# Performance work log

Measured on AMD Instinct MI355X. Metric: run time of the kernel, lower is better.

The kernel has to match this reference:

```python
import jax, jax.numpy as jnp
import numpy as np

SEQ_LEN = 256
HIDDEN = 1024
OUT = 512
BATCH = 256


def setup_inputs() -> dict:
    key = jax.random.key(0)
    ks = jax.random.split(key, 7)
    s_h = 1.0 / np.sqrt(HIDDEN)
    c_vector = jax.random.normal(ks[0], (BATCH, HIDDEN), dtype=jnp.float32)
    # PyTorch LSTMCell params: weight_ih (4H, I), weight_hh (4H, H), biases (4H)
    W_ih = jax.random.uniform(ks[1], (4 * HIDDEN, OUT), jnp.float32, -s_h, s_h)
    W_hh = jax.random.uniform(ks[2], (4 * HIDDEN, HIDDEN), jnp.float32, -s_h, s_h)
    b_ih = jax.random.uniform(ks[3], (4 * HIDDEN,), jnp.float32, -s_h, s_h)
    b_hh = jax.random.uniform(ks[4], (4 * HIDDEN,), jnp.float32, -s_h, s_h)
    W_out = jax.random.uniform(ks[5], (OUT, HIDDEN), jnp.float32, -s_h, s_h)
    b_out = jax.random.uniform(ks[6], (OUT,), jnp.float32, -s_h, s_h)
    return {"c_vector": c_vector, "W_ih": W_ih, "W_hh": W_hh, "b_ih": b_ih,
            "b_hh": b_hh, "W_out": W_out, "b_out": b_out}


def reference(c_vector, W_ih, W_hh, b_ih, b_hh, W_out, b_out):
    B = c_vector.shape[0]
    bias = b_ih + b_hh

    def step(carry, _):
        h, c, x = carry
        gates = x @ W_ih.T + h @ W_hh.T + bias  # (B, 4H)
        i, f, g, o = jnp.split(gates, 4, axis=-1)  # PyTorch gate order i,f,g,o
        c_new = jax.nn.sigmoid(f) * c + jax.nn.sigmoid(i) * jnp.tanh(g)
        h_new = jax.nn.sigmoid(o) * jnp.tanh(c_new)
        o_t = c_new @ W_out.T + b_out  # fc_out applied to cell state, per source
        return (h_new, c_new, o_t), (h_new, c_new, o_t)

    x0 = jnp.zeros((B, W_ih.shape[1]), dtype=c_vector.dtype)
    _, (hs, cs, outs) = jax.lax.scan(step, (c_vector, c_vector, x0), None, length=SEQ_LEN)
    # scan stacks on axis 0 (time); source returns (B, T, .)
    return (jnp.swapaxes(hs, 0, 1), jnp.swapaxes(cs, 0, 1), jnp.swapaxes(outs, 0, 1))
```

## Files before the change

### kernel.cpp

```cpp
#include <hip/hip_runtime.h>
#include <cstdint>
#include <cstddef>
#include <type_traits>


#define SEQ    256
#define BATCH  256
#define HID    1024
#define OUTD   512
#define KDIM   2048
#define GATES  4096

typedef __bf16 bf16x8 __attribute__((ext_vector_type(8)));
typedef float  f32x4  __attribute__((ext_vector_type(4)));

__device__ __forceinline__ unsigned short f2bf(float x) {
  unsigned u = __float_as_uint(x);
  u = (u + 0x7FFFu + ((u >> 16) & 1u)) >> 16;
  return (unsigned short)u;
}

__device__ __forceinline__ f32x4 mfma16(bf16x8 a, bf16x8 b, f32x4 c) {
  return __builtin_amdgcn_mfma_f32_16x16x32_bf16(a, b, c, 0, 0, 0);
}

__device__ __forceinline__ bf16x8 ld_frag_bf(const unsigned short* p) {
  uint4 u = *reinterpret_cast<const uint4*>(p);
  return __builtin_bit_cast(bf16x8, u);
}

__device__ __forceinline__ float rcp_fast(float x) {
  float r;
  asm("v_rcp_f32 %0, %1" : "=v"(r) : "v"(x));
  return r;
}
__device__ __forceinline__ float sigmoid_fast(float x) {
  return rcp_fast(1.f + __expf(-x));
}
__device__ __forceinline__ float tanh_fast(float x) {
  float xc = fminf(fmaxf(x, -15.f), 15.f);
  float e2 = __expf(2.f * xc);
  return 1.f - 2.f * rcp_fast(1.f + e2);
}

#define GLOAD_LDS16(gp, lp)                                                   \
  __builtin_amdgcn_global_load_lds(                                           \
      (const __attribute__((address_space(1))) unsigned int*)(gp),            \
      (__attribute__((address_space(3))) unsigned int*)(lp), 16, 0, 0)


__global__ void k_cast_whh(const float* __restrict__ whh, unsigned short* __restrict__ wg2) {
  int i4 = blockIdx.x * blockDim.x + threadIdx.x;
  if (i4 >= (GATES * HID) / 4) return;
  int idx = i4 * 4;
  int n = idx >> 10, k = idx & 1023;
  const float4 v = *reinterpret_cast<const float4*>(whh + idx);
  ushort4 o; o.x = f2bf(v.x); o.y = f2bf(v.y); o.z = f2bf(v.z); o.w = f2bf(v.w);
  *reinterpret_cast<ushort4*>(wg2 + (size_t)n * KDIM + k) = o;
}

__global__ void k_cast_wout(const float* __restrict__ wout,
                            unsigned short* __restrict__ wott) {
  int idx = blockIdx.x * blockDim.x + threadIdx.x;
  if (idx >= OUTD * HID) return;
  int j = idx >> 10, k = idx & 1023;
  wott[(size_t)k * OUTD + j] = f2bf(wout[idx]);
}

__global__ void k_init(const float* __restrict__ cvec,
                       unsigned short* __restrict__ a0,
                       unsigned* __restrict__ flags) {
  int idx = blockIdx.x * blockDim.x + threadIdx.x;
  if (idx < 256) flags[idx] = 0u;
  if (idx >= BATCH * KDIM) return;
  int b = idx >> 11, k = idx & 2047;
  a0[idx] = (k < HID) ? f2bf(cvec[(size_t)b * HID + k]) : (unsigned short)0;
}

__global__ void k_bias(const float* __restrict__ wih, const float* __restrict__ b_ih,
                       const float* __restrict__ b_hh, const float* __restrict__ b_out,
                       float* __restrict__ bias0, float* __restrict__ bias2) {
  int wave = threadIdx.x >> 6, l = threadIdx.x & 63;
  int n = blockIdx.x * 4 + wave;
  float s = 0.f;
  for (int j = l; j < OUTD; j += 64) s += wih[(size_t)n * OUTD + j] * b_out[j];
  for (int off = 32; off; off >>= 1) s += __shfl_down(s, off);
  if (l == 0) {
    float b0 = b_ih[n] + b_hh[n];
    bias0[n] = b0;
    bias2[n] = b0 + s;
  }
}

template <typename AT>
__device__ __forceinline__ bf16x8 ld_frag(const AT* p) {
  if constexpr (std::is_same_v<AT, float>) {
    const float4 f0 = *reinterpret_cast<const float4*>(p);
    const float4 f1 = *reinterpret_cast<const float4*>(p + 4);
    uint4 v;
    v.x = (unsigned)f2bf(f0.x) | ((unsigned)f2bf(f0.y) << 16);
    v.y = (unsigned)f2bf(f0.z) | ((unsigned)f2bf(f0.w) << 16);
    v.z = (unsigned)f2bf(f1.x) | ((unsigned)f2bf(f1.y) << 16);
    v.w = (unsigned)f2bf(f1.z) | ((unsigned)f2bf(f1.w) << 16);
    return __builtin_bit_cast(bf16x8, v);
  } else {
    return ld_frag_bf(p);
  }
}

template <typename AT, typename BT, typename DT, int F, int KC>
__global__ __launch_bounds__(256)
void k_gemm(const AT* __restrict__ A, int lda,
            const BT* __restrict__ Bn, int ldb,
            DT* __restrict__ D, int ldd,
            const float* __restrict__ bias, int K) {
  __shared__ char lds[F * 16 * KC * 2];
  const int tid = threadIdx.x;
  const int w = tid >> 6, l = tid & 63;
  const int n0 = blockIdx.x * (F * 16);
  const int m0 = blockIdx.y * 64 + w * 16;
  const int lr = l & 15, lg = l >> 4;

  f32x4 acc[F] = {};
  for (int kc = 0; kc < K; kc += KC) {
    __syncthreads();
#pragma unroll
    for (int it = 0; it < (F * 16 * (KC / 8)) / 256; ++it) {
      int idx = tid + it * 256;
      int col = idx / (KC / 8), k16 = idx % (KC / 8);
      uint4 v;
      if constexpr (std::is_same_v<BT, float>) {
        const float* src = Bn + (size_t)(n0 + col) * ldb + kc + k16 * 8;
        const float4 f0 = *reinterpret_cast<const float4*>(src);
        const float4 f1 = *reinterpret_cast<const float4*>(src + 4);
        v.x = (unsigned)f2bf(f0.x) | ((unsigned)f2bf(f0.y) << 16);
        v.y = (unsigned)f2bf(f0.z) | ((unsigned)f2bf(f0.w) << 16);
        v.z = (unsigned)f2bf(f1.x) | ((unsigned)f2bf(f1.y) << 16);
        v.w = (unsigned)f2bf(f1.z) | ((unsigned)f2bf(f1.w) << 16);
      } else {
        v = *reinterpret_cast<const uint4*>(Bn + (size_t)(n0 + col) * ldb + kc + k16 * 8);
      }
      int db = col * (KC * 2) + ((k16 * 16) ^ ((col & 7) << 4));
      *reinterpret_cast<uint4*>(lds + db) = v;
    }
    __syncthreads();
    const AT* Arow = A + (size_t)(m0 + lr) * lda + kc + lg * 8;
#pragma unroll
    for (int ks = 0; ks < KC / 32; ++ks) {
      bf16x8 af = ld_frag(Arow + ks * 32);
      int kb = ks * 64 + lg * 16;
#pragma unroll
      for (int f = 0; f < F; ++f) {
        int col = f * 16 + lr;
        uint4 u = *reinterpret_cast<const uint4*>(
            lds + col * (KC * 2) + (kb ^ ((col & 7) << 4)));
        acc[f] = mfma16(af, __builtin_bit_cast(bf16x8, u), acc[f]);
      }
    }
  }
#pragma unroll
  for (int f = 0; f < F; ++f) {
    int cg = n0 + f * 16 + lr;
    float bv = bias ? bias[cg] : 0.f;
#pragma unroll
    for (int j = 0; j < 4; ++j) {
      int r = m0 + lg * 4 + j;
      float val = acc[f][j] + bv;
      if constexpr (std::is_same_v<DT, unsigned short>) D[(size_t)r * ldd + cg] = f2bf(val);
      else                                              D[(size_t)r * ldd + cg] = val;
    }
  }
}

__global__ __launch_bounds__(512, 2)
void k_lstm_p5(unsigned short* __restrict__ Ab0,
               unsigned short* __restrict__ Ab1,
               const unsigned short* __restrict__ Wg2,
               const float* __restrict__ bias0,
               const float* __restrict__ bias2,
               const float* __restrict__ cvec,
               float* __restrict__ hs,
               float* __restrict__ cs,
               unsigned* __restrict__ flags) {
  __shared__ char lds[131072];
  const int tid = threadIdx.x;
  const int wave = tid >> 6, l = tid & 63;
  const int wn = wave >> 2, wk = wave & 3;
  const int bid = blockIdx.x;
  const int mg = (bid & 7) >> 1;
  const int ng = (bid >> 3) | ((bid & 1) << 5);
  const int lr = l & 15, lg = l >> 4;

  bf16x8 B[8][2][2];
#pragma unroll
  for (int c = 0; c < 8; ++c)
#pragma unroll
    for (int ks = 0; ks < 2; ++ks)
#pragma unroll
      for (int in = 0; in < 2; ++in) {
        int col = wn * 32 + in * 16 + lr;
        int grow = (col >> 4) * HID + ng * 16 + (col & 15);
        int kb = c * 256 + wk * 64 + ks * 32 + lg * 8;
        B[c][ks][in] = ld_frag_bf(Wg2 + (size_t)grow * KDIM + kb);
      }

  const int m = tid >> 3;
  const int hcp = tid & 7;
  const int b_row = mg * 64 + m;
  const int hid0 = ng * 16 + hcp * 2;
  float creg[2];
  {
    const float2 cv = *reinterpret_cast<const float2*>(cvec + (size_t)b_row * HID + hid0);
    creg[0] = cv.x; creg[1] = cv.y;
  }
  float b0r[2][4], b2r[2][4];
#pragma unroll
  for (int e = 0; e < 2; ++e)
#pragma unroll
    for (int g = 0; g < 4; ++g) {
      b0r[e][g] = bias0[g * HID + hid0 + e];
      b2r[e][g] = bias2[g * HID + hid0 + e];
    }
  asm volatile("s_waitcnt vmcnt(0)" ::: "memory");

  for (int t = 0; t < SEQ; ++t) {
    const unsigned short* Acur = (t & 1) ? Ab1 : Ab0;
    unsigned short* Anxt = (t & 1) ? Ab0 : Ab1;

    if (t > 0) {
      if (wave == 0) {
        for (;;) {
          unsigned v = __hip_atomic_load(&flags[(mg << 6) + l],
                                         __ATOMIC_RELAXED, __HIP_MEMORY_SCOPE_AGENT);
          if (__all((int)(v >= (unsigned)t))) break;
          __builtin_amdgcn_s_sleep(0);
        }
        (void)__hip_atomic_load(&flags[mg << 6], __ATOMIC_ACQUIRE,
                                __HIP_MEMORY_SCOPE_AGENT);
      }
      __syncthreads();
    }

    auto STAGE = [&](int buf, int c) {
      const unsigned short* base = Acur + (size_t)(mg * 64) * KDIM + c * 256;
#pragma unroll
      for (int it = 0; it < 4; ++it) {
        int s_lin = it * 512 + tid;
        int row = s_lin >> 5, slot = s_lin & 31;
        const unsigned short* g = base + (size_t)row * KDIM + ((slot ^ (row & 7)) * 8);
        GLOAD_LDS16(g, lds + buf * 32768 + s_lin * 16);
      }
    };

    STAGE(0, 0);
    STAGE(1, 1);
    STAGE(2, 2);

    f32x4 acc[4][2] = {};
#pragma unroll
    for (int c = 0; c < 8; ++c) {
      if (c <= 5)      { asm volatile("s_waitcnt vmcnt(8)" ::: "memory"); }
      else if (c == 6) { asm volatile("s_waitcnt vmcnt(4)" ::: "memory"); }
      else             { asm volatile("s_waitcnt vmcnt(0)" ::: "memory"); }
      __builtin_amdgcn_s_barrier();
      const char* buf = lds + (c & 3) * 32768;
#pragma unroll
      for (int ks = 0; ks < 2; ++ks) {
        bf16x8 a[4];
#pragma unroll
        for (int im = 0; im < 4; ++im) {
          int row = im * 16 + lr;
          int k16 = wk * 8 + ks * 4 + lg;
          a[im] = *reinterpret_cast<const bf16x8*>(
              buf + row * 512 + ((k16 ^ (row & 7)) << 4));
        }
#pragma unroll
        for (int im = 0; im < 4; ++im)
#pragma unroll
          for (int in = 0; in < 2; ++in)
            acc[im][in] = mfma16(a[im], B[c][ks][in], acc[im][in]);
      }
      if (c <= 4) STAGE((c + 3) & 3, c + 3);
    }

    asm volatile("" ::: "memory");
    __builtin_amdgcn_s_barrier();
#pragma unroll
    for (int im = 0; im < 4; ++im)
#pragma unroll
      for (int in = 0; in < 2; ++in)
        *reinterpret_cast<f32x4*>(lds + wave * 8704 + (im * 2 + in) * 1088
                                  + l * 16 + (l >> 4) * 16) = acc[im][in];
    __syncthreads();

    float cn2[2], hn2[2];
#pragma unroll
    for (int e = 0; e < 2; ++e) {
      int hc = hcp * 2 + e;
      float pre[4];
#pragma unroll
      for (int g = 0; g < 4; ++g) {
        int n = g * 16 + hc;
        int wn_r = n >> 5, nn = n & 31;
        int frag = ((m >> 4) << 1) | (nn >> 4);
        int lane_r = ((m & 15) >> 2) * 16 + (nn & 15);
        int j = m & 3;
        float s = 0.f;
#pragma unroll
        for (int wkk = 0; wkk < 4; ++wkk)
          s += *reinterpret_cast<const float*>(
              lds + (wn_r * 4 + wkk) * 8704 + frag * 1088
              + lane_r * 16 + ((m & 15) >> 2) * 16 + j * 4);
        pre[g] = s + ((t == 0) ? b0r[e][g] : b2r[e][g]);
      }
      float si = sigmoid_fast(pre[0]);
      float sf = sigmoid_fast(pre[1]);
      float so = sigmoid_fast(pre[3]);
      float tg = tanh_fast(pre[2]);
      float cn = sf * creg[e] + si * tg;
      float hn = so * tanh_fast(cn);
      creg[e] = cn;
      cn2[e] = cn;
      hn2[e] = hn;
    }
    unsigned hpack = (unsigned)f2bf(hn2[0]) | ((unsigned)f2bf(hn2[1]) << 16);
    unsigned cpack = (unsigned)f2bf(cn2[0]) | ((unsigned)f2bf(cn2[1]) << 16);
    __hip_atomic_store(reinterpret_cast<unsigned*>(Anxt + (size_t)b_row * KDIM + hid0),
                       hpack, __ATOMIC_RELAXED, __HIP_MEMORY_SCOPE_AGENT);
    __hip_atomic_store(reinterpret_cast<unsigned*>(Anxt + (size_t)b_row * KDIM + HID + hid0),
                       cpack, __ATOMIC_RELAXED, __HIP_MEMORY_SCOPE_AGENT);
    asm volatile("s_waitcnt vmcnt(0)" ::: "memory");
    __builtin_amdgcn_s_barrier();
    if (tid == 0)
      __hip_atomic_store(&flags[(mg << 6) + ng], (unsigned)(t + 1),
                         __ATOMIC_RELAXED, __HIP_MEMORY_SCOPE_AGENT);
    size_t o = (size_t)b_row * (SEQ * HID) + (size_t)t * HID + hid0;
    *reinterpret_cast<float2*>(hs + o) = make_float2(hn2[0], hn2[1]);
    *reinterpret_cast<float2*>(cs + o) = make_float2(cn2[0], cn2[1]);
  }
}

extern "C" void kernel_launch(void* const* d_in, const int* in_sizes, int n_in,
                              void* d_out, int out_size, void* d_ws, size_t ws_size,
                              hipStream_t stream) {
  const float* c_vec = (const float*)d_in[0];
  const float* W_ih  = (const float*)d_in[1];
  const float* W_hh  = (const float*)d_in[2];
  const float* b_ih  = (const float*)d_in[3];
  const float* b_hh  = (const float*)d_in[4];
  const float* W_out = (const float*)d_in[5];
  const float* b_out = (const float*)d_in[6];

  float* out = (float*)d_out;
  float* hs = out;
  float* cs = out + (size_t)BATCH * SEQ * HID;
  float* os = out + (size_t)2 * BATCH * SEQ * HID;

  char* sc = (char*)os;
  unsigned short* Wg2   = (unsigned short*)(sc);
  unsigned short* WoTT  = (unsigned short*)(sc + (16u << 20));
  unsigned short* A0    = (unsigned short*)(sc + (17u << 20));
  unsigned short* A1    = (unsigned short*)(sc + (18u << 20));
  float*          bias0 = (float*)(sc + (19u << 20));
  float*          bias2 = (float*)(sc + (19u << 20) + 16384);
  unsigned*       g_flg = (unsigned*)(sc + (19u << 20) + 32768);

  k_cast_whh<<<dim3(GATES * HID / 4 / 256), dim3(256), 0, stream>>>(W_hh, Wg2);
  k_cast_wout<<<dim3(OUTD * HID / 256), dim3(256), 0, stream>>>(W_out, WoTT);
  k_init<<<dim3(BATCH * KDIM / 256), dim3(256), 0, stream>>>(c_vec, A0, g_flg);
  k_bias<<<dim3(GATES / 4), dim3(256), 0, stream>>>(W_ih, b_ih, b_hh, b_out, bias0, bias2);
  k_gemm<float, unsigned short, unsigned short, 4, 512>
      <<<dim3(HID / 64, GATES / 64), dim3(256), 0, stream>>>(
      W_ih, OUTD, WoTT, OUTD, Wg2 + HID, KDIM, (const float*)nullptr, OUTD);

  {
    void* args[] = {(void*)&A0, (void*)&A1, (void*)&Wg2, (void*)&bias0,
                    (void*)&bias2, (void*)&c_vec, (void*)&hs, (void*)&cs,
                    (void*)&g_flg};
    hipLaunchCooperativeKernel((const void*)k_lstm_p5, dim3(256), dim3(512),
                               args, 0, stream);
  }

  k_gemm<float, float, float, 8, 256>
      <<<dim3(OUTD / 128, BATCH * SEQ / 64), dim3(256), 0, stream>>>(
      cs, HID, W_out, HID, os, OUTD, b_out, HID);
}
```

Before: 2.728 ms.

## Split per-step flag wait into four groups overlapped with K-chunk staging

The single spin-wait on all 64 producer flags at the start of each timestep is replaced by four partial polls, each waiting on 16 flags. After each poll the block stages the two K-chunks that depend on those producers (the recurrent-input and hidden parts), so loads and MFMA work can start before every producer block has finished the previous step. This adds extra __syncthreads per step and reorders the chunk pipeline, and it relies on the mapping from flag groups to K-chunks being correct.

```diff
diff --git a/kernel.cpp b/kernel.cpp
--- a/kernel.cpp
+++ b/kernel.cpp
@@ -173,7 +173,7 @@
 }
 
 __global__ __launch_bounds__(512, 2)
-void k_lstm_p5(unsigned short* __restrict__ Ab0,
+void k_lstm_p6(unsigned short* __restrict__ Ab0,
                unsigned short* __restrict__ Ab1,
                const unsigned short* __restrict__ Wg2,
                const float* __restrict__ bias0,
@@ -227,19 +227,20 @@
     const unsigned short* Acur = (t & 1) ? Ab1 : Ab0;
     unsigned short* Anxt = (t & 1) ? Ab0 : Ab1;
 
-    if (t > 0) {
-      if (wave == 0) {
+    auto POLL = [&](int g) {
+      if (t > 0 && wave == 0) {
         for (;;) {
-          unsigned v = __hip_atomic_load(&flags[(mg << 6) + l],
+          unsigned v = __hip_atomic_load(&flags[(mg << 6) + g * 16 + (l & 15)],
                                          __ATOMIC_RELAXED, __HIP_MEMORY_SCOPE_AGENT);
           if (__all((int)(v >= (unsigned)t))) break;
           __builtin_amdgcn_s_sleep(0);
         }
-        (void)__hip_atomic_load(&flags[mg << 6], __ATOMIC_ACQUIRE,
-                                __HIP_MEMORY_SCOPE_AGENT);
+        if (g == 0)
+          (void)__hip_atomic_load(&flags[mg << 6], __ATOMIC_ACQUIRE,
+                                  __HIP_MEMORY_SCOPE_AGENT);
       }
       __syncthreads();
-    }
+    };
 
     auto STAGE = [&](int buf, int c) {
       const unsigned short* base = Acur + (size_t)(mg * 64) * KDIM + c * 256;
@@ -252,18 +253,9 @@
       }
     };
 
-    STAGE(0, 0);
-    STAGE(1, 1);
-    STAGE(2, 2);
-
     f32x4 acc[4][2] = {};
-#pragma unroll
-    for (int c = 0; c < 8; ++c) {
-      if (c <= 5)      { asm volatile("s_waitcnt vmcnt(8)" ::: "memory"); }
-      else if (c == 6) { asm volatile("s_waitcnt vmcnt(4)" ::: "memory"); }
-      else             { asm volatile("s_waitcnt vmcnt(0)" ::: "memory"); }
-      __builtin_amdgcn_s_barrier();
-      const char* buf = lds + (c & 3) * 32768;
+    auto COMPUTE = [&](int buf, int c) {
+      const char* bp = lds + buf * 32768;
 #pragma unroll
       for (int ks = 0; ks < 2; ++ks) {
         bf16x8 a[4];
@@ -272,7 +264,7 @@
           int row = im * 16 + lr;
           int k16 = wk * 8 + ks * 4 + lg;
           a[im] = *reinterpret_cast<const bf16x8*>(
-              buf + row * 512 + ((k16 ^ (row & 7)) << 4));
+              bp + row * 512 + ((k16 ^ (row & 7)) << 4));
         }
 #pragma unroll
         for (int im = 0; im < 4; ++im)
@@ -280,8 +272,28 @@
           for (int in = 0; in < 2; ++in)
             acc[im][in] = mfma16(a[im], B[c][ks][in], acc[im][in]);
       }
-      if (c <= 4) STAGE((c + 3) & 3, c + 3);
-    }
+    };
+
+    POLL(0);
+    STAGE(0, 0); STAGE(1, 4);
+    POLL(1);
+    STAGE(2, 1); STAGE(3, 5);
+    asm volatile("s_waitcnt vmcnt(8)" ::: "memory");
+    __builtin_amdgcn_s_barrier();
+    COMPUTE(0, 0); COMPUTE(1, 4);
+    POLL(2);
+    STAGE(0, 2); STAGE(1, 6);
+    asm volatile("s_waitcnt vmcnt(8)" ::: "memory");
+    __builtin_amdgcn_s_barrier();
+    COMPUTE(2, 1); COMPUTE(3, 5);
+    POLL(3);
+    STAGE(2, 3); STAGE(3, 7);
+    asm volatile("s_waitcnt vmcnt(8)" ::: "memory");
+    __builtin_amdgcn_s_barrier();
+    COMPUTE(0, 2); COMPUTE(1, 6);
+    asm volatile("s_waitcnt vmcnt(0)" ::: "memory");
+    __builtin_amdgcn_s_barrier();
+    COMPUTE(2, 3); COMPUTE(3, 7);
 
     asm volatile("" ::: "memory");
     __builtin_amdgcn_s_barrier();
@@ -377,7 +389,7 @@
     void* args[] = {(void*)&A0, (void*)&A1, (void*)&Wg2, (void*)&bias0,
                     (void*)&bias2, (void*)&c_vec, (void*)&hs, (void*)&cs,
                     (void*)&g_flg};
-    hipLaunchCooperativeKernel((const void*)k_lstm_p5, dim3(256), dim3(512),
+    hipLaunchCooperativeKernel((const void*)k_lstm_p6, dim3(256), dim3(512),
                                args, 0, stream);
   }
 
```

Result: slower. 2.946 ms (+8.0%).

## Split recurrent GEMM K across all eight waves with four-gate fragments per wave

Applied to the files above, without the earlier changes.

Each wave of the persistent LSTM kernel now owns a 32-wide K slice and computes all four gate columns, instead of a 2x4 split over N and K. Each A fragment read from LDS now feeds four MFMAs instead of two, and the per-chunk LDS reads drop. The partial sums are laid out per row in LDS so the gate reduction becomes eight vectorized f32x4 loads instead of scattered scalar loads. In exchange the cross-wave reduction now covers 8 partials instead of 4, and LDS grows to 139264 bytes, which with launch bounds of 2 blocks may limit residency.

```diff
diff --git a/kernel.cpp b/kernel.cpp
--- a/kernel.cpp
+++ b/kernel.cpp
@@ -173,7 +173,7 @@
 }
 
 __global__ __launch_bounds__(512, 2)
-void k_lstm_p5(unsigned short* __restrict__ Ab0,
+void k_lstm_p7(unsigned short* __restrict__ Ab0,
                unsigned short* __restrict__ Ab1,
                const unsigned short* __restrict__ Wg2,
                const float* __restrict__ bias0,
@@ -182,27 +182,21 @@
                float* __restrict__ hs,
                float* __restrict__ cs,
                unsigned* __restrict__ flags) {
-  __shared__ char lds[131072];
+  __shared__ char lds[139264];
   const int tid = threadIdx.x;
   const int wave = tid >> 6, l = tid & 63;
-  const int wn = wave >> 2, wk = wave & 3;
   const int bid = blockIdx.x;
   const int mg = (bid & 7) >> 1;
   const int ng = (bid >> 3) | ((bid & 1) << 5);
   const int lr = l & 15, lg = l >> 4;
 
-  bf16x8 B[8][2][2];
+  bf16x8 B[8][4];
 #pragma unroll
   for (int c = 0; c < 8; ++c)
 #pragma unroll
-    for (int ks = 0; ks < 2; ++ks)
-#pragma unroll
-      for (int in = 0; in < 2; ++in) {
-        int col = wn * 32 + in * 16 + lr;
-        int grow = (col >> 4) * HID + ng * 16 + (col & 15);
-        int kb = c * 256 + wk * 64 + ks * 32 + lg * 8;
-        B[c][ks][in] = ld_frag_bf(Wg2 + (size_t)grow * KDIM + kb);
-      }
+    for (int g = 0; g < 4; ++g)
+      B[c][g] = ld_frag_bf(Wg2 + (size_t)(g * HID + ng * 16 + lr) * KDIM
+                           + c * 256 + wave * 32 + lg * 8);
 
   const int m = tid >> 3;
   const int hcp = tid & 7;
@@ -256,30 +250,27 @@
     STAGE(1, 1);
     STAGE(2, 2);
 
-    f32x4 acc[4][2] = {};
+    f32x4 acc[4][4] = {};
 #pragma unroll
     for (int c = 0; c < 8; ++c) {
       if (c <= 5)      { asm volatile("s_waitcnt vmcnt(8)" ::: "memory"); }
       else if (c == 6) { asm volatile("s_waitcnt vmcnt(4)" ::: "memory"); }
       else             { asm volatile("s_waitcnt vmcnt(0)" ::: "memory"); }
       __builtin_amdgcn_s_barrier();
-      const char* buf = lds + (c & 3) * 32768;
-#pragma unroll
-      for (int ks = 0; ks < 2; ++ks) {
-        bf16x8 a[4];
-#pragma unroll
-        for (int im = 0; im < 4; ++im) {
-          int row = im * 16 + lr;
-          int k16 = wk * 8 + ks * 4 + lg;
-          a[im] = *reinterpret_cast<const bf16x8*>(
-              buf + row * 512 + ((k16 ^ (row & 7)) << 4));
-        }
-#pragma unroll
-        for (int im = 0; im < 4; ++im)
-#pragma unroll
-          for (int in = 0; in < 2; ++in)
-            acc[im][in] = mfma16(a[im], B[c][ks][in], acc[im][in]);
-      }
+      const char* bp = lds + (c & 3) * 32768;
+      bf16x8 a[4];
+#pragma unroll
+      for (int im = 0; im < 4; ++im) {
+        int row = im * 16 + lr;
+        int s16 = wave * 4 + lg;
+        a[im] = *reinterpret_cast<const bf16x8*>(
+            bp + row * 512 + ((s16 ^ (row & 7)) << 4));
+      }
+#pragma unroll
+      for (int im = 0; im < 4; ++im)
+#pragma unroll
+        for (int g = 0; g < 4; ++g)
+          acc[im][g] = mfma16(a[im], B[c][g], acc[im][g]);
       if (c <= 4) STAGE((c + 3) & 3, c + 3);
     }
 
@@ -288,31 +279,27 @@
 #pragma unroll
     for (int im = 0; im < 4; ++im)
 #pragma unroll
-      for (int in = 0; in < 2; ++in)
-        *reinterpret_cast<f32x4*>(lds + wave * 8704 + (im * 2 + in) * 1088
-                                  + l * 16 + (l >> 4) * 16) = acc[im][in];
+      for (int j = 0; j < 4; ++j) {
+        f32x4 v;
+        v[0] = acc[im][0][j]; v[1] = acc[im][1][j];
+        v[2] = acc[im][2][j]; v[3] = acc[im][3][j];
+        int row = im * 16 + lg * 4 + j;
+        *reinterpret_cast<f32x4*>(lds + wave * 17408 + row * 272 + lr * 16) = v;
+      }
     __syncthreads();
 
     float cn2[2], hn2[2];
 #pragma unroll
     for (int e = 0; e < 2; ++e) {
       int hc = hcp * 2 + e;
+      f32x4 s = {};
+#pragma unroll
+      for (int w8 = 0; w8 < 8; ++w8)
+        s += *reinterpret_cast<const f32x4*>(lds + w8 * 17408 + m * 272 + hc * 16);
       float pre[4];
 #pragma unroll
-      for (int g = 0; g < 4; ++g) {
-        int n = g * 16 + hc;
-        int wn_r = n >> 5, nn = n & 31;
-        int frag = ((m >> 4) << 1) | (nn >> 4);
-        int lane_r = ((m & 15) >> 2) * 16 + (nn & 15);
-        int j = m & 3;
-        float s = 0.f;
-#pragma unroll
-        for (int wkk = 0; wkk < 4; ++wkk)
-          s += *reinterpret_cast<const float*>(
-              lds + (wn_r * 4 + wkk) * 8704 + frag * 1088
-              + lane_r * 16 + ((m & 15) >> 2) * 16 + j * 4);
-        pre[g] = s + ((t == 0) ? b0r[e][g] : b2r[e][g]);
-      }
+      for (int g = 0; g < 4; ++g)
+        pre[g] = s[g] + ((t == 0) ? b0r[e][g] : b2r[e][g]);
       float si = sigmoid_fast(pre[0]);
       float sf = sigmoid_fast(pre[1]);
       float so = sigmoid_fast(pre[3]);
@@ -377,7 +364,7 @@
     void* args[] = {(void*)&A0, (void*)&A1, (void*)&Wg2, (void*)&bias0,
                     (void*)&bias2, (void*)&c_vec, (void*)&hs, (void*)&cs,
                     (void*)&g_flg};
-    hipLaunchCooperativeKernel((const void*)k_lstm_p5, dim3(256), dim3(512),
+    hipLaunchCooperativeKernel((const void*)k_lstm_p7, dim3(256), dim3(512),
                                args, 0, stream);
   }
 
```

Result: slower. 3.159 ms (+15.8%).
